# Optimization experiments

Measured on AMD Instinct MI355X. Metric: run time of the kernel, lower is better.

## Reference

```python
import jax, jax.numpy as jnp
import numpy as np
from jax import lax

SOS_TOKEN = 0
PAD_LEN = 30  # tokenizer.pad_len -> number of greedy decode steps


def _gru_cell(x, h, w_ih, w_hh, b_ih, b_hh):
    # PyTorch GRU cell math. x,h: [B,H]; w_*: [3H,H]; b_*: [3H]
    gi = x @ w_ih.T + b_ih
    gh = h @ w_hh.T + b_hh
    i_r, i_z, i_n = jnp.split(gi, 3, axis=-1)
    h_r, h_z, h_n = jnp.split(gh, 3, axis=-1)
    r = jax.nn.sigmoid(i_r + h_r)
    z = jax.nn.sigmoid(i_z + h_z)
    n = jnp.tanh(i_n + r * h_n)
    return (1.0 - z) * n + z * h


def _sm_encode(sm_hidden, conv_w, conv_b, enc_w, enc_b):
    # sm_hidden: [B, L, C] -> conv over time with C input channels
    x = jnp.transpose(sm_hidden, (0, 2, 1))  # [B, C, L]
    conv = lax.conv_general_dilated(
        x, conv_w, window_strides=(1,), padding='VALID',
        dimension_numbers=('NCH', 'OIH', 'NCH'))  # [B, O, L-k+1]
    conv = jax.nn.relu(conv + conv_b[None, :, None])
    pooled = jnp.max(conv, axis=-1)  # [B, O]
    return jax.nn.relu(pooled @ enc_w.T + enc_b)  # [B, H]


def reference(sm_hidden, embedding, w_ih, w_hh, b_ih, b_hh,
              w_out, b_out, conv_w, conv_b, enc_w, enc_b):
    B = sm_hidden.shape[0]
    h0 = _sm_encode(sm_hidden, conv_w, conv_b, enc_w, enc_b)  # [B, H]

    # The original re-runs the GRU over the whole (append-only) prefix each
    # iteration; since the GRU is deterministic this equals incremental
    # single-step updates, which we do here.
    def step(carry, _):
        h, tok = carry
        emb = embedding[tok]                      # [B, H]
        h_new = _gru_cell(emb, h, w_ih, w_hh, b_ih, b_hh)
        logits = h_new @ w_out.T + b_out          # [B, V]
        tok_new = jnp.argmax(logits, axis=-1)     # greedy topk(1)
        return (h_new, tok_new), (h_new, tok_new)

    tok0 = jnp.full((B,), SOS_TOKEN, dtype=jnp.int32)
    (h_last, _), (hiddens, toks) = lax.scan(step, (h0, tok0), None, length=PAD_LEN)

    decoder_output = jax.nn.log_softmax(h_last @ w_out.T + b_out, axis=1)  # [B, V]
    decoder_hidden = hiddens  # [PAD_LEN, B, H] == rnn_out of final _base_forward
    decoded_indices = jnp.concatenate([tok0[None, :], toks], axis=0)  # [PAD_LEN+1, B]
    return decoder_output, decoder_hidden, decoded_indices


def setup_inputs() -> dict:
    key = jax.random.key(0)
    ks = jax.random.split(key, 12)
    B, L, C = 512, 120, 128
    H, V, O, K = 1024, 512, 32, 10
    s = 1.0 / np.sqrt(H)
    return {
        'sm_hidden': jax.random.normal(ks[0], (B, L, C), jnp.float32),
        'embedding': jax.random.normal(ks[1], (V, H), jnp.float32),
        'w_ih': jax.random.uniform(ks[2], (3 * H, H), jnp.float32, -s, s),
        'w_hh': jax.random.uniform(ks[3], (3 * H, H), jnp.float32, -s, s),
        'b_ih': jax.random.uniform(ks[4], (3 * H,), jnp.float32, -s, s),
        'b_hh': jax.random.uniform(ks[5], (3 * H,), jnp.float32, -s, s),
        'w_out': jax.random.uniform(ks[6], (V, H), jnp.float32, -s, s),
        'b_out': jax.random.uniform(ks[7], (V,), jnp.float32, -s, s),
        'conv_w': jax.random.normal(ks[8], (O, C, K), jnp.float32) * 0.05,
        'conv_b': jax.random.normal(ks[9], (O,), jnp.float32) * 0.05,
        'enc_w': jax.random.uniform(ks[10], (H, O), jnp.float32, -s, s),
        'enc_b': jax.random.uniform(ks[11], (H,), jnp.float32, -s, s),
    }
```

## Files before the change

### kernel.cpp

```cpp
#include <hip/hip_runtime.h>
#include <hip/hip_bf16.h>
#include <math.h>

#define Bsz 512
#define Hd 1024
#define Vd 512
#define Cc 128
#define Ll 120
#define Kk 10
#define Oo 32
#define NSTEP 30

typedef __attribute__((ext_vector_type(8))) short bf16x8;
typedef __attribute__((ext_vector_type(4))) float f32x4;
typedef unsigned short ushort;
typedef unsigned long long u64;

#define BARLDS() asm volatile("s_waitcnt lgkmcnt(0)\n\ts_barrier" ::: "memory")

static __device__ __forceinline__ float sigm(float x) { return 1.f / (1.f + expf(-x)); }
static __device__ __forceinline__ ushort f2bf(float x) {
    __hip_bfloat16 h = __float2bfloat16(x);
    return *(ushort*)&h;
}
static __device__ __forceinline__ float bf2f(ushort u) {
    __hip_bfloat16 h; *(ushort*)&h = u;
    return __bfloat162float(h);
}
static __device__ __forceinline__ unsigned monofy(float f) {
    unsigned u = __float_as_uint(f);
    return (u & 0x80000000u) ? ~u : (u | 0x80000000u);
}

__global__ void k_packall(const float* __restrict__ wih, ushort* __restrict__ wihH, ushort* __restrict__ wihL,
                          const float* __restrict__ whh, ushort* __restrict__ whhH, ushort* __restrict__ whhL,
                          const float* __restrict__ wout, ushort* __restrict__ woutH, ushort* __restrict__ woutL,
                          const float* __restrict__ emb, ushort* __restrict__ embH, ushort* __restrict__ embL) {
    int gidx = blockIdx.x * 256 + threadIdx.x;
    const float* W;
    ushort *hi, *lo;
    int idx;
    if (gidx < 3145728)      { W = wih;  hi = wihH;  lo = wihL;  idx = gidx; }
    else if (gidx < 6291456) { W = whh;  hi = whhH;  lo = whhL;  idx = gidx - 3145728; }
    else if (gidx < 6815744) { W = wout; hi = woutH; lo = woutL; idx = gidx - 6291456; }
    else if (gidx < 7340032) { W = emb;  hi = embH;  lo = embL;  idx = gidx - 6815744; }
    else return;
    int jj = idx & 7, l = (idx >> 3) & 63, c = (idx >> 9) & 31, nf = idx >> 14;
    int n = nf * 16 + (l & 15);
    int k = c * 32 + ((l >> 4) << 3) + jj;
    float v = W[(size_t)n * 1024 + k];
    ushort h = f2bf(v);
    hi[idx] = h;
    lo[idx] = f2bf(v - bf2f(h));
}

__global__ void k_packconv(const float* __restrict__ cw, ushort* __restrict__ hi,
                           ushort* __restrict__ lo) {
    int idx = blockIdx.x * 256 + threadIdx.x;
    if (idx >= 2 * 40 * 64 * 8) return;
    int jj = idx & 7, l = (idx >> 3) & 63, ch = (idx >> 9) % 40, nf = idx / (40 * 512);
    int o = nf * 16 + (l & 15);
    int k = ch * 32 + ((l >> 4) << 3) + jj;
    int kc = k >> 7, c = k & 127;
    float v = cw[(o * Cc + c) * Kk + kc];
    ushort h = f2bf(v);
    hi[idx] = h;
    lo[idx] = f2bf(v - bf2f(h));
}

__global__ __launch_bounds__(512) void k_convmfma(const float* __restrict__ sm,
                                                  const ushort* __restrict__ wH,
                                                  const ushort* __restrict__ wL,
                                                  const float* __restrict__ cb,
                                                  const float* __restrict__ ew,
                                                  const float* __restrict__ eb,
                                                  float* __restrict__ h0,
                                                  ushort* __restrict__ ApHi,
                                                  ushort* __restrict__ ApLo) {
    __shared__ ushort hiS[2][137 * 128];
    __shared__ ushort loS[2][137 * 128];
    __shared__ float sred[8][2][2][16];
    __shared__ float ps[2][Oo];
    int b0 = blockIdx.x * 2, tid = threadIdx.x, wid = tid >> 6, l = tid & 63;

    for (int i = tid; i < 3840; i += 512) {
        int s = i >= 1920;
        int local = i - s * 1920;
        int row = local >> 4, col0 = (local & 15) * 8;
        const float* smb = sm + (size_t)(b0 + s) * (Ll * Cc);
        float4 fa = *(const float4*)(smb + row * Cc + col0);
        float4 fb = *(const float4*)(smb + row * Cc + col0 + 4);
        float vv[8] = {fa.x, fa.y, fa.z, fa.w, fb.x, fb.y, fb.z, fb.w};
        ushort h8[8], l8[8];
#pragma unroll
        for (int q = 0; q < 8; ++q) {
            ushort h = f2bf(vv[q]);
            h8[q] = h;
            l8[q] = f2bf(vv[q] - bf2f(h));
        }
        int o = ((row << 8) + (col0 << 1)) ^ ((row & 7) << 4);
        *(bf16x8*)((char*)hiS[s] + o) = *(bf16x8*)h8;
        *(bf16x8*)((char*)loS[s] + o) = *(bf16x8*)l8;
    }
    __syncthreads();

    f32x4 acc[2][2];
#pragma unroll
    for (int s = 0; s < 2; ++s)
#pragma unroll
        for (int j = 0; j < 2; ++j) acc[s][j] = (f32x4)0.f;

    bf16x8 aH0[2], aL0[2], bH0[2], bL0[2];
    bf16x8 aH1[2], aL1[2], bH1[2], bL1[2];

#define CLD(AH, AL, BH, BL, ch)                                                        \
    {                                                                                  \
        int row = wid * 16 + (l & 15) + ((ch) >> 2);                                   \
        int o = ((row << 8) + ((((ch) & 3) * 32 + ((l >> 4) << 3)) << 1))              \
                ^ ((row & 7) << 4);                                                    \
        _Pragma("unroll") for (int s = 0; s < 2; ++s) {                                \
            AH[s] = *(const bf16x8*)((const char*)hiS[s] + o);                         \
            AL[s] = *(const bf16x8*)((const char*)loS[s] + o);                         \
        }                                                                              \
        _Pragma("unroll") for (int nf = 0; nf < 2; ++nf) {                             \
            int boff = ((nf * 40 + (ch)) * 64 + l) * 8;                                \
            BH[nf] = *(const bf16x8*)(wH + boff);                                      \
            BL[nf] = *(const bf16x8*)(wL + boff);                                      \
        }                                                                              \
    }
#define CST(AH, AL, BH, BL)                                                            \
    {                                                                                  \
        _Pragma("unroll") for (int s = 0; s < 2; ++s)                                  \
            _Pragma("unroll") for (int nf = 0; nf < 2; ++nf) {                         \
                acc[s][nf] = __builtin_amdgcn_mfma_f32_16x16x32_bf16(AH[s], BH[nf], acc[s][nf], 0, 0, 0); \
                acc[s][nf] = __builtin_amdgcn_mfma_f32_16x16x32_bf16(AH[s], BL[nf], acc[s][nf], 0, 0, 0); \
                acc[s][nf] = __builtin_amdgcn_mfma_f32_16x16x32_bf16(AL[s], BH[nf], acc[s][nf], 0, 0, 0); \
            }                                                                          \
    }

    CLD(aH0, aL0, bH0, bL0, 0)
#pragma unroll
    for (int ch = 0; ch < 40; ch += 2) {
        CLD(aH1, aL1, bH1, bL1, ch + 1)
        CST(aH0, aL0, bH0, bL0)
        if (ch + 2 < 40) CLD(aH0, aL0, bH0, bL0, ch + 2)
        CST(aH1, aL1, bH1, bL1)
    }
#undef CLD
#undef CST

    float mx[2][2] = {{-1e38f, -1e38f}, {-1e38f, -1e38f}};
    {
        int tb = wid * 16 + ((l >> 4) << 2);
#pragma unroll
        for (int q = 0; q < 4; ++q) {
            if (tb + q <= 110) {
#pragma unroll
                for (int s = 0; s < 2; ++s) {
                    mx[s][0] = fmaxf(mx[s][0], acc[s][0][q]);
                    mx[s][1] = fmaxf(mx[s][1], acc[s][1][q]);
                }
            }
        }
    }
#pragma unroll
    for (int sh = 16; sh < 64; sh <<= 1) {
#pragma unroll
        for (int s = 0; s < 2; ++s) {
            mx[s][0] = fmaxf(mx[s][0], __shfl_xor(mx[s][0], sh));
            mx[s][1] = fmaxf(mx[s][1], __shfl_xor(mx[s][1], sh));
        }
    }
    if (l < 16) {
#pragma unroll
        for (int s = 0; s < 2; ++s) {
            sred[wid][s][0][l] = mx[s][0];
            sred[wid][s][1][l] = mx[s][1];
        }
    }
    __syncthreads();
    if (tid < 64) {
        int s = tid >> 5, o = tid & 31;
        float m = sred[0][s][o >> 4][o & 15];
#pragma unroll
        for (int w = 1; w < 8; ++w) m = fmaxf(m, sred[w][s][o >> 4][o & 15]);
        ps[s][o] = fmaxf(m + cb[o], 0.f);
    }
    __syncthreads();
    for (int j = tid; j < Hd; j += 512) {
        const float4* e4 = (const float4*)(ew + (size_t)j * Oo);
        float4 w0 = e4[0], w1 = e4[1], w2 = e4[2], w3 = e4[3];
        float4 w4 = e4[4], w5 = e4[5], w6 = e4[6], w7 = e4[7];
        float ebj = eb[j];
        int c = j >> 5, sub = (j >> 3) & 3, jj = j & 7;
#pragma unroll
        for (int s = 0; s < 2; ++s) {
            int b = b0 + s;
            const float* p = ps[s];
            float a = ebj;
            a += p[0] * w0.x + p[1] * w0.y + p[2] * w0.z + p[3] * w0.w;
            a += p[4] * w1.x + p[5] * w1.y + p[6] * w1.z + p[7] * w1.w;
            a += p[8] * w2.x + p[9] * w2.y + p[10] * w2.z + p[11] * w2.w;
            a += p[12] * w3.x + p[13] * w3.y + p[14] * w3.z + p[15] * w3.w;
            a += p[16] * w4.x + p[17] * w4.y + p[18] * w4.z + p[19] * w4.w;
            a += p[20] * w5.x + p[21] * w5.y + p[22] * w5.z + p[23] * w5.w;
            a += p[24] * w6.x + p[25] * w6.y + p[26] * w6.z + p[27] * w6.w;
            a += p[28] * w7.x + p[29] * w7.y + p[30] * w7.z + p[31] * w7.w;
            a = fmaxf(a, 0.f);
            h0[(size_t)b * Hd + j] = a;
            ushort hb = f2bf(a);
            ushort lb = f2bf(a - bf2f(hb));
            int amf = b >> 4;
            int lane_r = (b & 15) + (sub << 4);
            int flat = ((amf * 32 + c) * 64 + lane_r) * 8 + jj;
            ApHi[flat] = hb;
            ApLo[flat] = lb;
        }
    }
}

template <int EPI>
__global__ __launch_bounds__(512, 2) void k_rnn(const ushort* __restrict__ Ah,
                                                const ushort* __restrict__ Al,
                                                const ushort* __restrict__ Bh,
                                                const ushort* __restrict__ Bl,
                                                const float* __restrict__ bias,
                                                float* __restrict__ outF,
                                                const float* __restrict__ gi_all,
                                                const u64* __restrict__ pkRd,
                                                u64* __restrict__ pkWr,
                                                float* __restrict__ outIdxRow,
                                                const float* __restrict__ hOld,
                                                ushort* __restrict__ ApHi,
                                                ushort* __restrict__ ApLo) {
    __shared__ ushort Bs[2][48][512];
    int id = blockIdx.x;
    int xcd = id & 7, r = id >> 3;
    int jt = xcd * 4 + (r & 3);
    int mt = r >> 2;
    int tid = threadIdx.x, wid = tid >> 6, l = tid & 63;
    int wm = wid >> 1, wj = wid & 1;
    int mf = mt * 4 + wm;
    int jf = jt * 2 + wj;
    int jcol = jf * 16 + (l & 15);

    float giR[4][3], hR[4];
    int bR[4], tkR[4];
    if constexpr (EPI == 1) {
#pragma unroll
        for (int q = 0; q < 4; ++q) {
            bR[q] = mf * 16 + ((l >> 4) << 2) + q;
            u64 pk = pkRd[bR[q]];
            tkR[q] = 511 - (int)(unsigned)(pk & 0xFFFFFFFFu);
            const float* gi = gi_all + (size_t)tkR[q] * 3072;
            giR[q][0] = gi[jcol];
            giR[q][1] = gi[1024 + jcol];
            giR[q][2] = gi[2048 + jcol];
            hR[q] = hOld[(size_t)bR[q] * 1024 + jcol];
        }
        if (jt == 0 && wj == 0 && (l & 15) == 0) {
#pragma unroll
            for (int q = 0; q < 4; ++q) {
                pkWr[bR[q]] = 0ULL;
                if (outIdxRow) outIdxRow[bR[q]] = (float)tkR[q];
            }
        }
    }

    f32x4 acc[3];
#pragma unroll
    for (int g = 0; g < 3; ++g) acc[g] = (f32x4)0.f;

    bf16x8 stg[6], aH0[4], aL0[4], aH1[4], aL1[4];

#define STG_LD(it)                                                                     \
    {                                                                                  \
        _Pragma("unroll") for (int k = 0; k < 6; ++k) {                                \
            int u = wid + 8 * k;                                                       \
            int hl = u & 1, wjb = (u >> 1) & 1, g = (u >> 2) % 3, cu = u / 12;         \
            const ushort* sp = hl ? Bl : Bh;                                           \
            stg[k] = *(const bf16x8*)(sp +                                             \
                (size_t)(((g * 64 + jt * 2 + wjb) * 32 + (it) * 4 + cu) * 64 + l) * 8);\
        }                                                                              \
    }
#define STG_WR(buf)                                                                    \
    {                                                                                  \
        _Pragma("unroll") for (int k = 0; k < 6; ++k)                                  \
            *(bf16x8*)&Bs[buf][wid + 8 * k][l * 8] = stg[k];                           \
    }
#define A_LD(DH, DL, it)                                                               \
    {                                                                                  \
        _Pragma("unroll") for (int cc = 0; cc < 4; ++cc) {                             \
            DH[cc] = *(const bf16x8*)(Ah + (size_t)((mf * 32 + (it) * 4 + cc) * 64 + l) * 8); \
            DL[cc] = *(const bf16x8*)(Al + (size_t)((mf * 32 + (it) * 4 + cc) * 64 + l) * 8); \
        }                                                                              \
    }
#define CMP(buf, AH, AL)                                                               \
    {                                                                                  \
        _Pragma("unroll") for (int cc = 0; cc < 4; ++cc)                               \
            _Pragma("unroll") for (int g = 0; g < 3; ++g) {                            \
                bf16x8 bhh = *(const bf16x8*)&Bs[buf][cc * 12 + g * 4 + wj * 2 + 0][l * 8]; \
                bf16x8 bll = *(const bf16x8*)&Bs[buf][cc * 12 + g * 4 + wj * 2 + 1][l * 8]; \
                acc[g] = __builtin_amdgcn_mfma_f32_16x16x32_bf16(AH[cc], bhh, acc[g], 0, 0, 0); \
                acc[g] = __builtin_amdgcn_mfma_f32_16x16x32_bf16(AH[cc], bll, acc[g], 0, 0, 0); \
                acc[g] = __builtin_amdgcn_mfma_f32_16x16x32_bf16(AL[cc], bhh, acc[g], 0, 0, 0); \
            }                                                                          \
    }

    STG_LD(0)
    STG_WR(0)
    STG_LD(1)
    A_LD(aH0, aL0, 0)
    BARLDS();
#pragma unroll
    for (int it = 0; it < 8; ++it) {
        int buf = it & 1;
        if (it < 7) STG_WR(buf ^ 1)
        if (it < 6) STG_LD(it + 2)
        if (it & 1) {
            if (it < 7) A_LD(aH0, aL0, it + 1)
            CMP(buf, aH1, aL1)
        } else {
            if (it < 7) A_LD(aH1, aL1, it + 1)
            CMP(buf, aH0, aL0)
        }
        BARLDS();
    }
#undef STG_LD
#undef STG_WR
#undef A_LD
#undef CMP

    if constexpr (EPI == 0) {
#pragma unroll
        for (int q = 0; q < 4; ++q) {
            int b = mf * 16 + ((l >> 4) << 2) + q;
#pragma unroll
            for (int g = 0; g < 3; ++g)
                outF[(size_t)b * 3072 + g * 1024 + jcol] =
                    acc[g][q] + bias[g * 1024 + jcol];
        }
    } else {
        float bj0 = bias[jcol], bj1 = bias[1024 + jcol], bj2 = bias[2048 + jcol];
        int c = jcol >> 5, sub = (jcol >> 3) & 3, jj = jcol & 7;
#pragma unroll
        for (int q = 0; q < 4; ++q) {
            int b = bR[q];
            float rr = sigm(giR[q][0] + acc[0][q] + bj0);
            float zz = sigm(giR[q][1] + acc[1][q] + bj1);
            float nn = tanhf(giR[q][2] + rr * (acc[2][q] + bj2));
            float hv = (1.f - zz) * nn + zz * hR[q];
            outF[(size_t)b * 1024 + jcol] = hv;
            ushort hb = f2bf(hv);
            ushort lb = f2bf(hv - bf2f(hb));
            int lane_r = (b & 15) + (sub << 4);
            int flat = (((b >> 4) * 32 + c) * 64 + lane_r) * 8 + jj;
            ApHi[flat] = hb;
            ApLo[flat] = lb;
        }
    }
}

__global__ __launch_bounds__(256) void k_lgt(const ushort* __restrict__ Ah,
                                             const ushort* __restrict__ Al,
                                             const ushort* __restrict__ Bh,
                                             const ushort* __restrict__ Bl,
                                             const float* __restrict__ bias,
                                             float* __restrict__ outF,
                                             u64* __restrict__ pkOut) {
    __shared__ ushort Bs[2][8][512];
    int id = blockIdx.x;
    int xcd = id & 7, r = id >> 3;
    int vf = xcd * 4 + (r & 3);
    int mg = r >> 2;
    int tid = threadIdx.x, w = tid >> 6, l = tid & 63;
    int mf = mg * 4 + w;

    f32x4 acc = (f32x4)0.f;
    bf16x8 stg[2];
    bf16x8 a0h[4], a0l[4], a1h[4], a1l[4];

#define LSTG_LD(it)                                                                    \
    {                                                                                  \
        _Pragma("unroll") for (int k = 0; k < 2; ++k) {                                \
            int s = tid + 256 * k;                                                     \
            int il = s & 63, u = s >> 6;                                               \
            int hl = u & 1, cu = u >> 1;                                               \
            const ushort* sp = hl ? Bl : Bh;                                           \
            stg[k] = *(const bf16x8*)(sp +                                             \
                (size_t)((vf * 32 + (it) * 4 + cu) * 64 + il) * 8);                    \
        }                                                                              \
    }
#define LSTG_WR(buf)                                                                   \
    {                                                                                  \
        _Pragma("unroll") for (int k = 0; k < 2; ++k) {                                \
            int s = tid + 256 * k;                                                     \
            int il = s & 63, u = s >> 6;                                               \
            *(bf16x8*)&Bs[buf][u][il * 8] = stg[k];                                    \
        }                                                                              \
    }
#define LA_LD(DH, DL, it)                                                              \
    {                                                                                  \
        _Pragma("unroll") for (int cu = 0; cu < 4; ++cu) {                             \
            size_t aoff = (size_t)((mf * 32 + (it) * 4 + cu) * 64 + l) * 8;            \
            DH[cu] = *(const bf16x8*)(Ah + aoff);                                      \
            DL[cu] = *(const bf16x8*)(Al + aoff);                                      \
        }                                                                              \
    }
#define LCMP(buf, AH, AL)                                                              \
    {                                                                                  \
        _Pragma("unroll") for (int cu = 0; cu < 4; ++cu) {                             \
            bf16x8 bh = *(const bf16x8*)&Bs[buf][cu * 2 + 0][l * 8];                   \
            bf16x8 bl = *(const bf16x8*)&Bs[buf][cu * 2 + 1][l * 8];                   \
            acc = __builtin_amdgcn_mfma_f32_16x16x32_bf16(AH[cu], bh, acc, 0, 0, 0);   \
            acc = __builtin_amdgcn_mfma_f32_16x16x32_bf16(AH[cu], bl, acc, 0, 0, 0);   \
            acc = __builtin_amdgcn_mfma_f32_16x16x32_bf16(AL[cu], bh, acc, 0, 0, 0);   \
        }                                                                              \
    }

    LSTG_LD(0)
    LSTG_WR(0)
    LSTG_LD(1)
    LA_LD(a0h, a0l, 0)
    BARLDS();
#pragma unroll
    for (int it = 0; it < 8; ++it) {
        int buf = it & 1;
        if (it < 7) LSTG_WR(buf ^ 1)
        if (it < 6) LSTG_LD(it + 2)
        if (it & 1) {
            if (it < 7) LA_LD(a0h, a0l, it + 1)
            LCMP(buf, a1h, a1l)
        } else {
            if (it < 7) LA_LD(a1h, a1l, it + 1)
            LCMP(buf, a0h, a0l)
        }
        BARLDS();
    }
#undef LSTG_LD
#undef LSTG_WR
#undef LA_LD
#undef LCMP

    int v = vf * 16 + (l & 15);
    float bv = bias[v];
    float lg[4];
    unsigned vmq[4];
#pragma unroll
    for (int q = 0; q < 4; ++q) {
        int b = mf * 16 + ((l >> 4) << 2) + q;
        lg[q] = acc[q] + bv;
        if (outF) outF[(size_t)b * Vd + v] = lg[q];
        vmq[q] = 511u - (unsigned)v;
    }
#pragma unroll
    for (int off = 1; off < 16; off <<= 1) {
#pragma unroll
        for (int q = 0; q < 4; ++q) {
            float og = __shfl_xor(lg[q], off);
            unsigned ov = __shfl_xor(vmq[q], off);
            if (og > lg[q] || (og == lg[q] && ov > vmq[q])) { lg[q] = og; vmq[q] = ov; }
        }
    }
    if ((l & 15) == 0) {
#pragma unroll
        for (int q = 0; q < 4; ++q) {
            int b = mf * 16 + ((l >> 4) << 2) + q;
            u64 pk = ((u64)monofy(lg[q]) << 32) | (u64)vmq[q];
            atomicMax(&pkOut[b], pk);
        }
    }
}

__global__ __launch_bounds__(64) void k_fin(const float* __restrict__ logits,
                                            const u64* __restrict__ pk,
                                            float* __restrict__ out_lsm,
                                            float* __restrict__ outIdxRow) {
    int b = blockIdx.x, l = threadIdx.x;
    const float* row = logits + (size_t)b * Vd;
    float bv = -3.4e38f;
#pragma unroll
    for (int s = 0; s < 8; ++s) bv = fmaxf(bv, row[s * 64 + l]);
#pragma unroll
    for (int off = 1; off < 64; off <<= 1) bv = fmaxf(bv, __shfl_xor(bv, off));
    float sum = 0.f;
#pragma unroll
    for (int s = 0; s < 8; ++s) sum += expf(row[s * 64 + l] - bv);
#pragma unroll
    for (int off = 1; off < 64; off <<= 1) sum += __shfl_xor(sum, off);
    float lse = logf(sum) + bv;
#pragma unroll
    for (int s = 0; s < 8; ++s) {
        int v = s * 64 + l;
        out_lsm[(size_t)b * Vd + v] = row[v] - lse;
    }
    if (l == 0)
        outIdxRow[b] = (float)(511 - (int)(unsigned)(pk[b] & 0xFFFFFFFFu));
}

__global__ void k_init(u64* __restrict__ P0, float* __restrict__ out_idx0) {
    int i = blockIdx.x * 64 + threadIdx.x;
    if (i < Bsz) {
        P0[i] = (1ULL << 32) | 511ULL;
        out_idx0[i] = 0.f;
    }
}

extern "C" void kernel_launch(void* const* d_in, const int* in_sizes, int n_in,
                              void* d_out, int out_size, void* d_ws, size_t ws_size,
                              hipStream_t stream) {
    const float* sm    = (const float*)d_in[0];
    const float* emb   = (const float*)d_in[1];
    const float* w_ih  = (const float*)d_in[2];
    const float* w_hh  = (const float*)d_in[3];
    const float* b_ih  = (const float*)d_in[4];
    const float* b_hh  = (const float*)d_in[5];
    const float* w_out = (const float*)d_in[6];
    const float* b_out = (const float*)d_in[7];
    const float* cw    = (const float*)d_in[8];
    const float* cb    = (const float*)d_in[9];
    const float* ew    = (const float*)d_in[10];
    const float* eb    = (const float*)d_in[11];

    float* out0 = (float*)d_out;
    float* out1 = out0 + (size_t)Bsz * Vd;
    float* out2 = out1 + (size_t)NSTEP * Bsz * Hd;

    char* wsp = (char*)d_ws;
    float*  f_gi  = (float*)wsp;  wsp += sizeof(float) * Bsz * 3072;
    float*  f_h0  = (float*)wsp;  wsp += sizeof(float) * Bsz * Hd;
    float*  f_log = (float*)wsp;  wsp += sizeof(float) * Bsz * Vd;
    u64*    Ppk0  = (u64*)wsp;    wsp += sizeof(u64) * Bsz;
    u64*    Ppk1  = (u64*)wsp;    wsp += sizeof(u64) * Bsz;
    ushort* ApHi0 = (ushort*)wsp; wsp += sizeof(ushort) * Bsz * Hd;
    ushort* ApLo0 = (ushort*)wsp; wsp += sizeof(ushort) * Bsz * Hd;
    ushort* ApHi1 = (ushort*)wsp; wsp += sizeof(ushort) * Bsz * Hd;
    ushort* ApLo1 = (ushort*)wsp; wsp += sizeof(ushort) * Bsz * Hd;
    ushort* embH  = (ushort*)wsp; wsp += sizeof(ushort) * Vd * Hd;
    ushort* embL  = (ushort*)wsp; wsp += sizeof(ushort) * Vd * Hd;
    ushort* wihH  = (ushort*)wsp; wsp += sizeof(ushort) * 3072 * Hd;
    ushort* wihL  = (ushort*)wsp; wsp += sizeof(ushort) * 3072 * Hd;
    ushort* whhH  = (ushort*)wsp; wsp += sizeof(ushort) * 3072 * Hd;
    ushort* whhL  = (ushort*)wsp; wsp += sizeof(ushort) * 3072 * Hd;
    ushort* woutH = (ushort*)wsp; wsp += sizeof(ushort) * Vd * Hd;
    ushort* woutL = (ushort*)wsp; wsp += sizeof(ushort) * Vd * Hd;
    ushort* cwBH  = (ushort*)wsp; wsp += sizeof(ushort) * 2 * 40 * 64 * 8;
    ushort* cwBL  = (ushort*)wsp; wsp += sizeof(ushort) * 2 * 40 * 64 * 8;

    k_packconv<<<160, 256, 0, stream>>>(cw, cwBH, cwBL);
    k_packall<<<(7340032 + 255) / 256, 256, 0, stream>>>(
        w_ih, wihH, wihL, w_hh, whhH, whhL, w_out, woutH, woutL, emb, embH, embL);
    k_convmfma<<<256, 512, 0, stream>>>(sm, cwBH, cwBL, cb, ew, eb,
                                        f_h0, ApHi0, ApLo0);
    k_rnn<0><<<256, 512, 0, stream>>>(embH, embL, wihH, wihL, b_ih, f_gi,
                                      nullptr, nullptr, nullptr, nullptr, nullptr,
                                      nullptr, nullptr);
    k_init<<<8, 64, 0, stream>>>(Ppk0, out2);

    ushort* aH[2] = {ApHi0, ApHi1};
    ushort* aL[2] = {ApLo0, ApLo1};
    u64* P[2] = {Ppk0, Ppk1};
    for (int t = 0; t < NSTEP; ++t) {
        int cur = t & 1, nxt = cur ^ 1;
        const float* hOld = (t == 0) ? f_h0 : (out1 + (size_t)(t - 1) * Bsz * Hd);
        k_rnn<1><<<256, 512, 0, stream>>>(
            aH[cur], aL[cur], whhH, whhL, b_hh, out1 + (size_t)t * Bsz * Hd,
            f_gi, P[t & 1], P[(t + 1) & 1],
            (t >= 1) ? (out2 + (size_t)t * Bsz) : nullptr,
            hOld, aH[nxt], aL[nxt]);
        k_lgt<<<256, 256, 0, stream>>>(aH[nxt], aL[nxt], woutH, woutL, b_out,
                                       (t == NSTEP - 1) ? f_log : nullptr,
                                       P[(t + 1) & 1]);
    }
    k_fin<<<Bsz, 64, 0, stream>>>(f_log, P[NSTEP & 1], out0,
                                  out2 + (size_t)NSTEP * Bsz);
}
```

Baseline: 767.1 us.

## Fuse GRU step and logits argmax into one kernel with a grid barrier

Merges the per-step recurrent GEMM with its GRU epilogue and the output-logits GEMM with its argmax into one kernel. A global atomic counter acts as a grid-wide barrier so every block can see the new hidden state before the logits phase starts. This removes one launch per decode step and its inter-kernel gap. In exchange, all 256 blocks must be co-resident, or the spin barrier deadlocks. The logits GEMM now loads A and B directly from global memory, split in K across wave pairs and reduced through LDS. The gather of gi and the old hidden state is also moved after the prologue loads so it overlaps with them.

```diff
diff --git a/kernel.cpp b/kernel.cpp
--- a/kernel.cpp
+++ b/kernel.cpp
@@ -219,20 +219,12 @@
     }
 }
 
-template <int EPI>
-__global__ __launch_bounds__(512, 2) void k_rnn(const ushort* __restrict__ Ah,
-                                                const ushort* __restrict__ Al,
-                                                const ushort* __restrict__ Bh,
-                                                const ushort* __restrict__ Bl,
-                                                const float* __restrict__ bias,
-                                                float* __restrict__ outF,
-                                                const float* __restrict__ gi_all,
-                                                const u64* __restrict__ pkRd,
-                                                u64* __restrict__ pkWr,
-                                                float* __restrict__ outIdxRow,
-                                                const float* __restrict__ hOld,
-                                                ushort* __restrict__ ApHi,
-                                                ushort* __restrict__ ApLo) {
+__global__ __launch_bounds__(512, 2) void k_gi(const ushort* __restrict__ Ah,
+                                               const ushort* __restrict__ Al,
+                                               const ushort* __restrict__ Bh,
+                                               const ushort* __restrict__ Bl,
+                                               const float* __restrict__ bias,
+                                               float* __restrict__ outF) {
     __shared__ ushort Bs[2][48][512];
     int id = blockIdx.x;
     int xcd = id & 7, r = id >> 3;
@@ -244,29 +236,6 @@
     int jf = jt * 2 + wj;
     int jcol = jf * 16 + (l & 15);
 
-    float giR[4][3], hR[4];
-    int bR[4], tkR[4];
-    if constexpr (EPI == 1) {
-#pragma unroll
-        for (int q = 0; q < 4; ++q) {
-            bR[q] = mf * 16 + ((l >> 4) << 2) + q;
-            u64 pk = pkRd[bR[q]];
-            tkR[q] = 511 - (int)(unsigned)(pk & 0xFFFFFFFFu);
-            const float* gi = gi_all + (size_t)tkR[q] * 3072;
-            giR[q][0] = gi[jcol];
-            giR[q][1] = gi[1024 + jcol];
-            giR[q][2] = gi[2048 + jcol];
-            hR[q] = hOld[(size_t)bR[q] * 1024 + jcol];
-        }
-        if (jt == 0 && wj == 0 && (l & 15) == 0) {
-#pragma unroll
-            for (int q = 0; q < 4; ++q) {
-                pkWr[bR[q]] = 0ULL;
-                if (outIdxRow) outIdxRow[bR[q]] = (float)tkR[q];
-            }
-        }
-    }
-
     f32x4 acc[3];
 #pragma unroll
     for (int g = 0; g < 3; ++g) acc[g] = (f32x4)0.f;
@@ -331,16 +300,131 @@
 #undef A_LD
 #undef CMP
 
-    if constexpr (EPI == 0) {
+#pragma unroll
+    for (int q = 0; q < 4; ++q) {
+        int b = mf * 16 + ((l >> 4) << 2) + q;
+#pragma unroll
+        for (int g = 0; g < 3; ++g)
+            outF[(size_t)b * 3072 + g * 1024 + jcol] = acc[g][q] + bias[g * 1024 + jcol];
+    }
+}
+
+__global__ __launch_bounds__(512, 2) void k_step(const ushort* __restrict__ Ah,
+                                                 const ushort* __restrict__ Al,
+                                                 const ushort* __restrict__ Bh,
+                                                 const ushort* __restrict__ Bl,
+                                                 const float* __restrict__ bias,
+                                                 float* __restrict__ outF,
+                                                 const float* __restrict__ gi_all,
+                                                 const u64* __restrict__ pkRd,
+                                                 u64* __restrict__ pkWr,
+                                                 float* __restrict__ outIdxRow,
+                                                 const float* __restrict__ hOld,
+                                                 ushort* __restrict__ ApHi,
+                                                 ushort* __restrict__ ApLo,
+                                                 const ushort* __restrict__ Wh,
+                                                 const ushort* __restrict__ Wl,
+                                                 const float* __restrict__ bout,
+                                                 float* __restrict__ f_log,
+                                                 int* __restrict__ cnt) {
+    __shared__ ushort Bs[2][48][512];
+    int id = blockIdx.x;
+    int xcd = id & 7, r = id >> 3;
+    int jt = xcd * 4 + (r & 3);
+    int mt = r >> 2;
+    int tid = threadIdx.x, wid = tid >> 6, l = tid & 63;
+    int wm = wid >> 1, wj = wid & 1;
+    int mf = mt * 4 + wm;
+    int jf = jt * 2 + wj;
+    int jcol = jf * 16 + (l & 15);
+
+    f32x4 acc[3];
+#pragma unroll
+    for (int g = 0; g < 3; ++g) acc[g] = (f32x4)0.f;
+
+    bf16x8 stg[6], aH0[4], aL0[4], aH1[4], aL1[4];
+
+#define STG_LD(it)                                                                     \
+    {                                                                                  \
+        _Pragma("unroll") for (int k = 0; k < 6; ++k) {                                \
+            int u = wid + 8 * k;                                                       \
+            int hl = u & 1, wjb = (u >> 1) & 1, g = (u >> 2) % 3, cu = u / 12;         \
+            const ushort* sp = hl ? Bl : Bh;                                           \
+            stg[k] = *(const bf16x8*)(sp +                                             \
+                (size_t)(((g * 64 + jt * 2 + wjb) * 32 + (it) * 4 + cu) * 64 + l) * 8);\
+        }                                                                              \
+    }
+#define STG_WR(buf)                                                                    \
+    {                                                                                  \
+        _Pragma("unroll") for (int k = 0; k < 6; ++k)                                  \
+            *(bf16x8*)&Bs[buf][wid + 8 * k][l * 8] = stg[k];                           \
+    }
+#define A_LD(DH, DL, it)                                                               \
+    {                                                                                  \
+        _Pragma("unroll") for (int cc = 0; cc < 4; ++cc) {                             \
+            DH[cc] = *(const bf16x8*)(Ah + (size_t)((mf * 32 + (it) * 4 + cc) * 64 + l) * 8); \
+            DL[cc] = *(const bf16x8*)(Al + (size_t)((mf * 32 + (it) * 4 + cc) * 64 + l) * 8); \
+        }                                                                              \
+    }
+#define CMP(buf, AH, AL)                                                               \
+    {                                                                                  \
+        _Pragma("unroll") for (int cc = 0; cc < 4; ++cc)                               \
+            _Pragma("unroll") for (int g = 0; g < 3; ++g) {                            \
+                bf16x8 bhh = *(const bf16x8*)&Bs[buf][cc * 12 + g * 4 + wj * 2 + 0][l * 8]; \
+                bf16x8 bll = *(const bf16x8*)&Bs[buf][cc * 12 + g * 4 + wj * 2 + 1][l * 8]; \
+                acc[g] = __builtin_amdgcn_mfma_f32_16x16x32_bf16(AH[cc], bhh, acc[g], 0, 0, 0); \
+                acc[g] = __builtin_amdgcn_mfma_f32_16x16x32_bf16(AH[cc], bll, acc[g], 0, 0, 0); \
+                acc[g] = __builtin_amdgcn_mfma_f32_16x16x32_bf16(AL[cc], bhh, acc[g], 0, 0, 0); \
+            }                                                                          \
+    }
+
+    STG_LD(0)
+    STG_WR(0)
+    STG_LD(1)
+    A_LD(aH0, aL0, 0)
+
+    float giR[4][3], hR[4];
+    int bR[4], tkR[4];
+#pragma unroll
+    for (int q = 0; q < 4; ++q) {
+        bR[q] = mf * 16 + ((l >> 4) << 2) + q;
+        u64 pk = pkRd[bR[q]];
+        tkR[q] = 511 - (int)(unsigned)(pk & 0xFFFFFFFFu);
+        const float* gi = gi_all + (size_t)tkR[q] * 3072;
+        giR[q][0] = gi[jcol];
+        giR[q][1] = gi[1024 + jcol];
+        giR[q][2] = gi[2048 + jcol];
+        hR[q] = hOld[(size_t)bR[q] * 1024 + jcol];
+    }
+    if (jt == 0 && wj == 0 && (l & 15) == 0) {
 #pragma unroll
         for (int q = 0; q < 4; ++q) {
-            int b = mf * 16 + ((l >> 4) << 2) + q;
-#pragma unroll
-            for (int g = 0; g < 3; ++g)
-                outF[(size_t)b * 3072 + g * 1024 + jcol] =
-                    acc[g][q] + bias[g * 1024 + jcol];
-        }
-    } else {
+            pkWr[bR[q]] = 0ULL;
+            if (outIdxRow) outIdxRow[bR[q]] = (float)tkR[q];
+        }
+    }
+
+    BARLDS();
+#pragma unroll
+    for (int it = 0; it < 8; ++it) {
+        int buf = it & 1;
+        if (it < 7) STG_WR(buf ^ 1)
+        if (it < 6) STG_LD(it + 2)
+        if (it & 1) {
+            if (it < 7) A_LD(aH0, aL0, it + 1)
+            CMP(buf, aH1, aL1)
+        } else {
+            if (it < 7) A_LD(aH1, aL1, it + 1)
+            CMP(buf, aH0, aL0)
+        }
+        BARLDS();
+    }
+#undef STG_LD
+#undef STG_WR
+#undef A_LD
+#undef CMP
+
+    {
         float bj0 = bias[jcol], bj1 = bias[1024 + jcol], bj2 = bias[2048 + jcol];
         int c = jcol >> 5, sub = (jcol >> 3) & 3, jj = jcol & 7;
 #pragma unroll
@@ -359,115 +443,80 @@
             ApLo[flat] = lb;
         }
     }
-}
-
-__global__ __launch_bounds__(256) void k_lgt(const ushort* __restrict__ Ah,
-                                             const ushort* __restrict__ Al,
-                                             const ushort* __restrict__ Bh,
-                                             const ushort* __restrict__ Bl,
-                                             const float* __restrict__ bias,
-                                             float* __restrict__ outF,
-                                             u64* __restrict__ pkOut) {
-    __shared__ ushort Bs[2][8][512];
-    int id = blockIdx.x;
-    int xcd = id & 7, r = id >> 3;
-    int vf = xcd * 4 + (r & 3);
-    int mg = r >> 2;
-    int tid = threadIdx.x, w = tid >> 6, l = tid & 63;
-    int mf = mg * 4 + w;
-
-    f32x4 acc = (f32x4)0.f;
-    bf16x8 stg[2];
-    bf16x8 a0h[4], a0l[4], a1h[4], a1l[4];
-
-#define LSTG_LD(it)                                                                    \
-    {                                                                                  \
-        _Pragma("unroll") for (int k = 0; k < 2; ++k) {                                \
-            int s = tid + 256 * k;                                                     \
-            int il = s & 63, u = s >> 6;                                               \
-            int hl = u & 1, cu = u >> 1;                                               \
-            const ushort* sp = hl ? Bl : Bh;                                           \
-            stg[k] = *(const bf16x8*)(sp +                                             \
-                (size_t)((vf * 32 + (it) * 4 + cu) * 64 + il) * 8);                    \
-        }                                                                              \
-    }
-#define LSTG_WR(buf)                                                                   \
-    {                                                                                  \
-        _Pragma("unroll") for (int k = 0; k < 2; ++k) {                                \
-            int s = tid + 256 * k;                                                     \
-            int il = s & 63, u = s >> 6;                                               \
-            *(bf16x8*)&Bs[buf][u][il * 8] = stg[k];                                    \
-        }                                                                              \
-    }
-#define LA_LD(DH, DL, it)                                                              \
-    {                                                                                  \
-        _Pragma("unroll") for (int cu = 0; cu < 4; ++cu) {                             \
-            size_t aoff = (size_t)((mf * 32 + (it) * 4 + cu) * 64 + l) * 8;            \
-            DH[cu] = *(const bf16x8*)(Ah + aoff);                                      \
-            DL[cu] = *(const bf16x8*)(Al + aoff);                                      \
-        }                                                                              \
-    }
-#define LCMP(buf, AH, AL)                                                              \
-    {                                                                                  \
-        _Pragma("unroll") for (int cu = 0; cu < 4; ++cu) {                             \
-            bf16x8 bh = *(const bf16x8*)&Bs[buf][cu * 2 + 0][l * 8];                   \
-            bf16x8 bl = *(const bf16x8*)&Bs[buf][cu * 2 + 1][l * 8];                   \
-            acc = __builtin_amdgcn_mfma_f32_16x16x32_bf16(AH[cu], bh, acc, 0, 0, 0);   \
-            acc = __builtin_amdgcn_mfma_f32_16x16x32_bf16(AH[cu], bl, acc, 0, 0, 0);   \
-            acc = __builtin_amdgcn_mfma_f32_16x16x32_bf16(AL[cu], bh, acc, 0, 0, 0);   \
-        }                                                                              \
-    }
-
-    LSTG_LD(0)
-    LSTG_WR(0)
-    LSTG_LD(1)
-    LA_LD(a0h, a0l, 0)
-    BARLDS();
-#pragma unroll
-    for (int it = 0; it < 8; ++it) {
-        int buf = it & 1;
-        if (it < 7) LSTG_WR(buf ^ 1)
-        if (it < 6) LSTG_LD(it + 2)
-        if (it & 1) {
-            if (it < 7) LA_LD(a0h, a0l, it + 1)
-            LCMP(buf, a1h, a1l)
-        } else {
-            if (it < 7) LA_LD(a1h, a1l, it + 1)
-            LCMP(buf, a0h, a0l)
-        }
-        BARLDS();
-    }
-#undef LSTG_LD
-#undef LSTG_WR
-#undef LA_LD
-#undef LCMP
-
-    int v = vf * 16 + (l & 15);
-    float bv = bias[v];
-    float lg[4];
-    unsigned vmq[4];
-#pragma unroll
-    for (int q = 0; q < 4; ++q) {
-        int b = mf * 16 + ((l >> 4) << 2) + q;
-        lg[q] = acc[q] + bv;
-        if (outF) outF[(size_t)b * Vd + v] = lg[q];
-        vmq[q] = 511u - (unsigned)v;
-    }
-#pragma unroll
-    for (int off = 1; off < 16; off <<= 1) {
+
+    __threadfence();
+    __syncthreads();
+    if (tid == 0) {
+        atomicAdd(cnt, 1);
+        while (__hip_atomic_load(cnt, __ATOMIC_ACQUIRE, __HIP_MEMORY_SCOPE_AGENT) < 256)
+            __builtin_amdgcn_s_sleep(1);
+    }
+    __syncthreads();
+
+    int q2 = wid >> 1, kh = wid & 1;
+    int mf2 = mt * 4 + q2;
+    int vf = jt;
+    f32x4 acc2 = (f32x4)0.f;
+    {
+        bf16x8 p0[4], p1[4];
+#define P2LD(P, c)                                                                     \
+    {                                                                                  \
+        size_t ao = (size_t)((mf2 * 32 + kh * 16 + (c)) * 64 + l) * 8;                 \
+        size_t bo = (size_t)((vf * 32 + kh * 16 + (c)) * 64 + l) * 8;                  \
+        P[0] = *(const bf16x8*)(ApHi + ao);                                            \
+        P[1] = *(const bf16x8*)(ApLo + ao);                                            \
+        P[2] = *(const bf16x8*)(Wh + bo);                                              \
+        P[3] = *(const bf16x8*)(Wl + bo);                                              \
+    }
+#define P2ST(P)                                                                        \
+    {                                                                                  \
+        acc2 = __builtin_amdgcn_mfma_f32_16x16x32_bf16(P[0], P[2], acc2, 0, 0, 0);     \
+        acc2 = __builtin_amdgcn_mfma_f32_16x16x32_bf16(P[0], P[3], acc2, 0, 0, 0);     \
+        acc2 = __builtin_amdgcn_mfma_f32_16x16x32_bf16(P[1], P[2], acc2, 0, 0, 0);     \
+    }
+        P2LD(p0, 0)
+#pragma unroll
+        for (int c = 0; c < 16; c += 2) {
+            P2LD(p1, c + 1)
+            P2ST(p0)
+            if (c + 2 < 16) P2LD(p0, c + 2)
+            P2ST(p1)
+        }
+#undef P2LD
+#undef P2ST
+    }
+    f32x4* red = (f32x4*)&Bs[0][0][0];
+    if (kh == 1) red[q2 * 64 + l] = acc2;
+    __syncthreads();
+    if (kh == 0) {
+        acc2 += red[q2 * 64 + l];
+        int v = vf * 16 + (l & 15);
+        float bv = bout[v];
+        float lg[4];
+        unsigned vmq[4];
 #pragma unroll
         for (int q = 0; q < 4; ++q) {
-            float og = __shfl_xor(lg[q], off);
-            unsigned ov = __shfl_xor(vmq[q], off);
-            if (og > lg[q] || (og == lg[q] && ov > vmq[q])) { lg[q] = og; vmq[q] = ov; }
-        }
-    }
-    if ((l & 15) == 0) {
-#pragma unroll
-        for (int q = 0; q < 4; ++q) {
-            int b = mf * 16 + ((l >> 4) << 2) + q;
-            u64 pk = ((u64)monofy(lg[q]) << 32) | (u64)vmq[q];
-            atomicMax(&pkOut[b], pk);
+            int b = mf2 * 16 + ((l >> 4) << 2) + q;
+            lg[q] = acc2[q] + bv;
+            if (f_log) f_log[(size_t)b * Vd + v] = lg[q];
+            vmq[q] = 511u - (unsigned)v;
+        }
+#pragma unroll
+        for (int off = 1; off < 16; off <<= 1) {
+#pragma unroll
+            for (int q = 0; q < 4; ++q) {
+                float og = __shfl_xor(lg[q], off);
+                unsigned ov = __shfl_xor(vmq[q], off);
+                if (og > lg[q] || (og == lg[q] && ov > vmq[q])) { lg[q] = og; vmq[q] = ov; }
+            }
+        }
+        if ((l & 15) == 0) {
+#pragma unroll
+            for (int q = 0; q < 4; ++q) {
+                int b = mf2 * 16 + ((l >> 4) << 2) + q;
+                u64 pk = ((u64)monofy(lg[q]) << 32) | (u64)vmq[q];
+                atomicMax(&pkWr[b], pk);
+            }
         }
     }
 }
@@ -498,12 +547,14 @@
         outIdxRow[b] = (float)(511 - (int)(unsigned)(pk[b] & 0xFFFFFFFFu));
 }
 
-__global__ void k_init(u64* __restrict__ P0, float* __restrict__ out_idx0) {
+__global__ void k_init(u64* __restrict__ P0, float* __restrict__ out_idx0,
+                       int* __restrict__ cnts) {
     int i = blockIdx.x * 64 + threadIdx.x;
     if (i < Bsz) {
         P0[i] = (1ULL << 32) | 511ULL;
         out_idx0[i] = 0.f;
     }
+    if (i < 32) cnts[i] = 0;
 }
 
 extern "C" void kernel_launch(void* const* d_in, const int* in_sizes, int n_in,
@@ -532,6 +583,7 @@
     float*  f_log = (float*)wsp;  wsp += sizeof(float) * Bsz * Vd;
     u64*    Ppk0  = (u64*)wsp;    wsp += sizeof(u64) * Bsz;
     u64*    Ppk1  = (u64*)wsp;    wsp += sizeof(u64) * Bsz;
+    int*    cnts  = (int*)wsp;    wsp += sizeof(int) * 32;
     ushort* ApHi0 = (ushort*)wsp; wsp += sizeof(ushort) * Bsz * Hd;
     ushort* ApLo0 = (ushort*)wsp; wsp += sizeof(ushort) * Bsz * Hd;
     ushort* ApHi1 = (ushort*)wsp; wsp += sizeof(ushort) * Bsz * Hd;
@@ -552,10 +604,8 @@
         w_ih, wihH, wihL, w_hh, whhH, whhL, w_out, woutH, woutL, emb, embH, embL);
     k_convmfma<<<256, 512, 0, stream>>>(sm, cwBH, cwBL, cb, ew, eb,
                                         f_h0, ApHi0, ApLo0);
-    k_rnn<0><<<256, 512, 0, stream>>>(embH, embL, wihH, wihL, b_ih, f_gi,
-                                      nullptr, nullptr, nullptr, nullptr, nullptr,
-                                      nullptr, nullptr);
-    k_init<<<8, 64, 0, stream>>>(Ppk0, out2);
+    k_gi<<<256, 512, 0, stream>>>(embH, embL, wihH, wihL, b_ih, f_gi);
+    k_init<<<8, 64, 0, stream>>>(Ppk0, out2, cnts);
 
     ushort* aH[2] = {ApHi0, ApHi1};
     ushort* aL[2] = {ApLo0, ApLo1};
@@ -563,14 +613,14 @@
     for (int t = 0; t < NSTEP; ++t) {
         int cur = t & 1, nxt = cur ^ 1;
         const float* hOld = (t == 0) ? f_h0 : (out1 + (size_t)(t - 1) * Bsz * Hd);
-        k_rnn<1><<<256, 512, 0, stream>>>(
+        k_step<<<256, 512, 0, stream>>>(
             aH[cur], aL[cur], whhH, whhL, b_hh, out1 + (size_t)t * Bsz * Hd,
-            f_gi, P[t & 1], P[(t + 1) & 1],
+            f_gi, P[cur], P[nxt],
             (t >= 1) ? (out2 + (size_t)t * Bsz) : nullptr,
-            hOld, aH[nxt], aL[nxt]);
-        k_lgt<<<256, 256, 0, stream>>>(aH[nxt], aL[nxt], woutH, woutL, b_out,
-                                       (t == NSTEP - 1) ? f_log : nullptr,
-                                       P[(t + 1) & 1]);
+            hOld, aH[nxt], aL[nxt],
+            woutH, woutL, b_out,
+            (t == NSTEP - 1) ? f_log : nullptr,
+            cnts + t);
     }
     k_fin<<<Bsz, 64, 0, stream>>>(f_log, P[NSTEP & 1], out0,
                                   out2 + (size_t)NSTEP * Bsz);
```

Measured after the change: 2.754 ms. 259% more time.
